# Performance work log

Hardware: AMD Instinct MI355X
Metric: run time of the kernel (lower is better)

The kernel has to match this reference:

```python
import jax, jax.numpy as jnp
import numpy as np

K = 4            # number of expert kernels
TEMPERATURE = 30.0  # T_max, initial temperature
KS = 3
PAD = 1
STRIDE = 1


def setup_inputs() -> dict:
    key = jax.random.key(0)
    k1, k2, k3, k4, k5 = jax.random.split(key, 5)
    b, c_in, c_out, f, t, ctx = 32, 256, 256, 64, 64, 256
    x = jax.random.normal(k1, (b, c_in, f, t), dtype=jnp.float32)
    g = jax.random.normal(k2, (b, ctx), dtype=jnp.float32)
    # expert kernels: (k, out, in//groups, ks, ks), kaiming-normal-ish init
    fan_in = c_in * KS * KS
    weight = jax.random.normal(k3, (K, c_out, c_in, KS, KS), dtype=jnp.float32) * jnp.sqrt(2.0 / fan_in)
    # attention Dense: ctx -> k * att_groups (att_groups = 1)
    dense_w = jax.random.normal(k4, (ctx, K), dtype=jnp.float32) * jnp.sqrt(1.0 / ctx)
    dense_b = jnp.zeros((K,), dtype=jnp.float32)
    return {"x": x, "g": g, "weight": weight, "dense_w": dense_w, "dense_b": dense_b}


def reference(x, g, weight, dense_w, dense_b):
    b, c, f, t = x.shape
    k, c_out, c_in_pg, ks, _ = weight.shape
    # attention over k expert kernels, per batch element (att_groups = 1)
    logits = g @ dense_w + dense_b                      # (b, k)
    attention = jax.nn.softmax(logits / TEMPERATURE, axis=-1)
    # per-sample mixed kernel: (b, out, in, ks, ks)
    agg_w = jnp.einsum('bk,koihw->boihw', attention, weight)
    agg_w = agg_w.reshape(b * c_out, c_in_pg, ks, ks)
    # batched per-sample conv via feature_group_count = groups * b (groups = 1)
    xg = x.reshape(1, b * c, f, t)
    out = jax.lax.conv_general_dilated(
        xg, agg_w,
        window_strides=(STRIDE, STRIDE),
        padding=((PAD, PAD), (PAD, PAD)),
        lhs_dilation=(1, 1), rhs_dilation=(1, 1),
        dimension_numbers=('NCHW', 'OIHW', 'NCHW'),
        feature_group_count=b,
    )
    return out.reshape(b, c_out, out.shape[-2], out.shape[-1])
```

## Files before the change

kernel.cpp:

```cpp
#include <hip/hip_runtime.h>
#include <hip/hip_bf16.h>
#include <stdint.h>

#define BATCH 32
#define CIN   256
#define COUT  256
#define FH    64
#define FW    64
#define NK    4
#define CTX   256
#define TEMP  30.0f

typedef __attribute__((ext_vector_type(8))) short bf16x8;
typedef __attribute__((ext_vector_type(4))) float f32x4;

__device__ __forceinline__ unsigned short f2bf(float f) {
    union { float f; uint32_t u; } a; a.f = f;
    uint32_t r = a.u + 0x7fffu + ((a.u >> 16) & 1u);
    return (unsigned short)(r >> 16);
}

#define WMIX_OFF  1024
#define WMIX_BYTES (32u * 9u * 8u * 4u * 256u * 16u)
#define XP_OFF    (WMIX_OFF + WMIX_BYTES)

__global__ void attn_kernel(const float* __restrict__ g,
                            const float* __restrict__ dw,
                            const float* __restrict__ db,
                            float* __restrict__ att) {
    int tid = threadIdx.x;
    int b = tid >> 2;
    int k = tid & 3;
    float acc = db[k];
    const float* gp = g + b * CTX;
    for (int i = 0; i < CTX; ++i)
        acc += gp[i] * dw[i * NK + k];
    acc *= (1.0f / TEMP);
    float m = acc;
    m = fmaxf(m, __shfl_xor(m, 1));
    m = fmaxf(m, __shfl_xor(m, 2));
    float e = expf(acc - m);
    float s = e;
    s += __shfl_xor(s, 1);
    s += __shfl_xor(s, 2);
    att[b * NK + k] = e / s;
}

__global__ __launch_bounds__(256, 2) void mix_kernel(
        const float* __restrict__ weight,
        const float* __restrict__ att,
        uint32_t* __restrict__ wmix) {
    __shared__ __align__(16) short S[2 * 8 * 2308];

    const int t   = threadIdx.x;
    const int cog = blockIdx.x;
    const int bg  = blockIdx.y;
    const int co0 = cog * 8;
    const int b0  = bg * 2;
    const size_t EST = (size_t)COUT * CIN * 9;

    float a[2][4];
#pragma unroll
    for (int nb = 0; nb < 2; ++nb)
#pragma unroll
        for (int k = 0; k < 4; ++k)
            a[nb][k] = att[(b0 + nb) * 4 + k];

    const int co_l  = t >> 5;
    const int inner = t & 31;
    const float* wbase = weight + (size_t)(co0 + co_l) * 2304;

#pragma unroll 2
    for (int i = 0; i < 18; ++i) {
        const int e4 = inner + 32 * i;
        float4 w[4];
#pragma unroll
        for (int k = 0; k < 4; ++k)
            w[k] = *(const float4*)(wbase + k * EST + (size_t)e4 * 4);
#pragma unroll
        for (int nb = 0; nb < 2; ++nb) {
            float mx = a[nb][0] * w[0].x + a[nb][1] * w[1].x + a[nb][2] * w[2].x + a[nb][3] * w[3].x;
            float my = a[nb][0] * w[0].y + a[nb][1] * w[1].y + a[nb][2] * w[2].y + a[nb][3] * w[3].y;
            float mz = a[nb][0] * w[0].z + a[nb][1] * w[1].z + a[nb][2] * w[2].z + a[nb][3] * w[3].z;
            float mw = a[nb][0] * w[0].w + a[nb][1] * w[1].w + a[nb][2] * w[2].w + a[nb][3] * w[3].w;
            uint32_t lo = (uint32_t)f2bf(mx) | ((uint32_t)f2bf(my) << 16);
            uint32_t hi = (uint32_t)f2bf(mz) | ((uint32_t)f2bf(mw) << 16);
            uint2* d = (uint2*)(S + ((nb * 8 + co_l) * 2308 + e4 * 4));
            *d = make_uint2(lo, hi);
        }
    }
    __syncthreads();

    const int co_w = t & 7;
    const int slot = t >> 3;
#pragma unroll 2
    for (int j = 0; j < 18; ++j) {
        const int GG  = j * 32 + slot;
        const int b_l = (GG >= 288) ? 1 : 0;
        const int rem = GG - b_l * 288;
        const int tap = rem >> 5;
        const int ch  = (rem >> 2) & 7;
        const int q   = rem & 3;
        const short* sp = S + (b_l * 8 + co_w) * 2308;
        const int ebase = (ch * 32 + q * 8) * 9 + tap;
        uint32_t d[4];
#pragma unroll
        for (int rp = 0; rp < 4; ++rp) {
            uint32_t lo = (uint16_t)sp[ebase + (2 * rp) * 9];
            uint32_t hi = (uint16_t)sp[ebase + (2 * rp + 1) * 9];
            d[rp] = lo | (hi << 16);
        }
        uint32_t* dst = wmix +
            ((((size_t)((b0 + b_l) * 9 + tap) * 8 + ch) * 4 + q) * 256 + co0 + co_w) * 4;
        *(uint4*)dst = make_uint4(d[0], d[1], d[2], d[3]);
    }
}

__global__ void xpad_kernel(const float* __restrict__ x,
                            uint32_t* __restrict__ xp) {
    __shared__ uint32_t P[1088];
    const int t  = threadIdx.x;
    const int y  = blockIdx.x;
    const int ch = blockIdx.y;
    const int b  = blockIdx.z;

    for (int i = t; i < 1088; i += 256) P[i] = 0;
    __syncthreads();

    if (y >= 1 && y <= 64) {
        const int ci_l = t >> 3;
        const int col0 = (t & 7) * 8;
        const float* xr = x + (((size_t)(b * 256 + ch * 32 + ci_l) * 64) + (y - 1)) * 64 + col0;
        float4 v0 = *(const float4*)xr;
        float4 v1 = *(const float4*)(xr + 4);
        unsigned short bf[8];
        bf[0] = f2bf(v0.x); bf[1] = f2bf(v0.y); bf[2] = f2bf(v0.z); bf[3] = f2bf(v0.w);
        bf[4] = f2bf(v1.x); bf[5] = f2bf(v1.y); bf[6] = f2bf(v1.z); bf[7] = f2bf(v1.w);
        const int q = ci_l >> 3, r = ci_l & 7;
        unsigned short* Ps = (unsigned short*)P;
#pragma unroll
        for (int j = 0; j < 8; ++j)
            Ps[(q * 68 + (col0 + j + 1)) * 8 + r] = bf[j];
    }
    __syncthreads();

    const int q = t >> 6, l = t & 63;
    uint32_t* base = xp + (((((size_t)(b * 8 + ch) * 4 + q) * 66) + y) * 68) * 4;
#pragma unroll
    for (int i = 0; i < 4; ++i)
        base[l + i * 64] = P[q * 272 + l + i * 64];
    if (l < 16) base[l + 256] = P[q * 272 + l + 256];
}

__global__ __launch_bounds__(256, 3) void conv_mfma(
        const char* __restrict__ xp,
        const char* __restrict__ wmix,
        float* __restrict__ out) {
    __shared__ __align__(16) short As[3 * 4 * 128 * 8];
    __shared__ __align__(16) short Bs[4 * 2 * 68 * 8];

    const int tid  = threadIdx.x;
    const int lane = tid & 63;
    const int wv   = tid >> 6;
    const int wm   = wv & 1;
    const int wn   = wv >> 1;
    const int l4   = lane >> 4;
    const int m16  = lane & 15;

    const int ptile = blockIdx.x;
    const int coT   = blockIdx.y;
    const int b     = blockIdx.z;
    const int y0    = ptile * 2;

    const char* wmix_b = wmix + (size_t)b * 9 * 8 * 4 * 256 * 16;
    const char* xp_b   = xp + (size_t)b * 8 * 4 * 66 * 68 * 16;

    f32x4 acc[4][4];
#pragma unroll
    for (int i = 0; i < 4; ++i)
#pragma unroll
        for (int j = 0; j < 4; ++j)
            acc[i][j] = (f32x4){0.f, 0.f, 0.f, 0.f};

    const int aLane = l4 * 2048 + wm * 1024 + m16 * 16;
    const int bLane = l4 * 2176 + wn * 1088 + m16 * 16;

#pragma unroll 1
    for (int ch = 0; ch < 8; ++ch) {
#pragma unroll 1
        for (int dy = 0; dy < 3; ++dy) {
            __syncthreads();
#pragma unroll
            for (int i = 0; i < 6; ++i) {
                const int s  = wv + i * 4;
                const int dx = s >> 3;
                const int q  = (s >> 1) & 3;
                const int h  = s & 1;
                const char* gsrc = wmix_b
                    + ((size_t)((dy * 3 + dx) * 8 + ch) * 4 + q) * 4096
                    + (coT * 128 + h * 64 + lane) * 16;
                char* ldst = (char*)As + ((dx * 4 + q) * 128 + h * 64 + lane) * 16;
                __builtin_amdgcn_global_load_lds(
                    (const __attribute__((address_space(1))) void*)gsrc,
                    (__attribute__((address_space(3))) void*)ldst, 16, 0, 0);
            }
            {
                const int yb = y0 + dy;
                const char* gsrc = xp_b
                    + (((size_t)ch * 4 + wv) * 66 + yb) * 1088 + lane * 16;
                char* ldst = (char*)Bs + wv * 2176 + lane * 16;
                __builtin_amdgcn_global_load_lds(
                    (const __attribute__((address_space(1))) void*)gsrc,
                    (__attribute__((address_space(3))) void*)ldst, 16, 0, 0);
                __builtin_amdgcn_global_load_lds(
                    (const __attribute__((address_space(1))) void*)(gsrc + 1024),
                    (__attribute__((address_space(3))) void*)(ldst + 1024), 16, 0, 0);
                if (lane < 8)
                    __builtin_amdgcn_global_load_lds(
                        (const __attribute__((address_space(1))) void*)(gsrc + 2048),
                        (__attribute__((address_space(3))) void*)(ldst + 2048), 16, 0, 0);
            }
            __syncthreads();

#pragma unroll
            for (int dx = 0; dx < 3; ++dx) {
                bf16x8 a[4], bb[4];
#pragma unroll
                for (int sm = 0; sm < 4; ++sm)
                    a[sm] = *(const bf16x8*)((const char*)As + dx * 8192 + aLane + sm * 256);
#pragma unroll
                for (int sn = 0; sn < 4; ++sn)
                    bb[sn] = *(const bf16x8*)((const char*)Bs + bLane + dx * 16 + sn * 256);
#pragma unroll
                for (int sm = 0; sm < 4; ++sm)
#pragma unroll
                    for (int sn = 0; sn < 4; ++sn)
                        acc[sm][sn] = __builtin_amdgcn_mfma_f32_16x16x32_bf16(
                            a[sm], bb[sn], acc[sm][sn], 0, 0, 0);
            }
        }
    }

    const int y = y0 + wn;
#pragma unroll
    for (int sm = 0; sm < 4; ++sm) {
#pragma unroll
        for (int sn = 0; sn < 4; ++sn) {
#pragma unroll
            for (int r = 0; r < 4; ++r) {
                const int co = coT * 128 + wm * 64 + sm * 16 + l4 * 4 + r;
                const int xx = sn * 16 + m16;
                out[(((size_t)b * COUT + co) * FH + y) * FW + xx] = acc[sm][sn][r];
            }
        }
    }
}

extern "C" void kernel_launch(void* const* d_in, const int* in_sizes, int n_in,
                              void* d_out, int out_size, void* d_ws, size_t ws_size,
                              hipStream_t stream) {
    const float* x       = (const float*)d_in[0];
    const float* g       = (const float*)d_in[1];
    const float* weight  = (const float*)d_in[2];
    const float* dense_w = (const float*)d_in[3];
    const float* dense_b = (const float*)d_in[4];
    float* out = (float*)d_out;

    float*    att  = (float*)d_ws;
    uint32_t* wmix = (uint32_t*)((char*)d_ws + WMIX_OFF);
    uint32_t* xp   = (uint32_t*)((char*)d_ws + XP_OFF);

    attn_kernel<<<1, 128, 0, stream>>>(g, dense_w, dense_b, att);
    mix_kernel<<<dim3(32, 16), 256, 0, stream>>>(weight, att, wmix);
    xpad_kernel<<<dim3(66, 8, BATCH), 256, 0, stream>>>(x, xp);

    dim3 grid(32, 2, BATCH);
    conv_mfma<<<grid, 256, 0, stream>>>((const char*)xp, (const char*)wmix, out);
}
```

Baseline: 401.4 us.

## Double-buffer conv LDS staging, fuse attention into mix, batch xpad rows, remap grid

The conv kernel now double-buffers its A and B LDS tiles, prefetching the next (channel, dy) stage while MFMAs run on the current one. It also pads LDS rows to avoid bank conflicts, raises MFMA priority with setprio, and swizzles the block index across XCDs. The attention softmax is recomputed inside each mix block, which removes one launch, and xpad handles six rows per block. In exchange, double buffering doubles LDS use, so launch bounds drop from 3 to 2 blocks per SM, which lowers occupancy.

```diff
diff --git a/kernel.cpp b/kernel.cpp
--- a/kernel.cpp
+++ b/kernel.cpp
@@ -24,33 +24,15 @@
 #define WMIX_BYTES (32u * 9u * 8u * 4u * 256u * 16u)
 #define XP_OFF    (WMIX_OFF + WMIX_BYTES)
 
-__global__ void attn_kernel(const float* __restrict__ g,
-                            const float* __restrict__ dw,
-                            const float* __restrict__ db,
-                            float* __restrict__ att) {
-    int tid = threadIdx.x;
-    int b = tid >> 2;
-    int k = tid & 3;
-    float acc = db[k];
-    const float* gp = g + b * CTX;
-    for (int i = 0; i < CTX; ++i)
-        acc += gp[i] * dw[i * NK + k];
-    acc *= (1.0f / TEMP);
-    float m = acc;
-    m = fmaxf(m, __shfl_xor(m, 1));
-    m = fmaxf(m, __shfl_xor(m, 2));
-    float e = expf(acc - m);
-    float s = e;
-    s += __shfl_xor(s, 1);
-    s += __shfl_xor(s, 2);
-    att[b * NK + k] = e / s;
-}
-
 __global__ __launch_bounds__(256, 2) void mix_kernel(
         const float* __restrict__ weight,
-        const float* __restrict__ att,
+        const float* __restrict__ g,
+        const float* __restrict__ dw,
+        const float* __restrict__ db,
         uint32_t* __restrict__ wmix) {
     __shared__ __align__(16) short S[2 * 8 * 2308];
+    __shared__ float logit_s[8];
+    __shared__ float att_s[8];
 
     const int t   = threadIdx.x;
     const int cog = blockIdx.x;
@@ -59,12 +41,44 @@
     const int b0  = bg * 2;
     const size_t EST = (size_t)COUT * CIN * 9;
 
+    {
+        const int p  = t >> 5;
+        const int i0 = t & 31;
+        const int nb = p >> 2, k = p & 3;
+        const float* gp = g + (size_t)(b0 + nb) * CTX;
+        float part = 0.f;
+#pragma unroll
+        for (int j = 0; j < 8; ++j) {
+            const int i = i0 + j * 32;
+            part += gp[i] * dw[i * NK + k];
+        }
+#pragma unroll
+        for (int m = 1; m <= 16; m <<= 1) part += __shfl_xor(part, m);
+        if (i0 == 0) logit_s[p] = part + db[k];
+    }
+    __syncthreads();
+    if (t < 8) {
+        const int nb = t >> 2;
+        const float l0 = logit_s[nb * 4 + 0] * (1.f / TEMP);
+        const float l1 = logit_s[nb * 4 + 1] * (1.f / TEMP);
+        const float l2 = logit_s[nb * 4 + 2] * (1.f / TEMP);
+        const float l3 = logit_s[nb * 4 + 3] * (1.f / TEMP);
+        const float m  = fmaxf(fmaxf(l0, l1), fmaxf(l2, l3));
+        const float e0 = expf(l0 - m), e1 = expf(l1 - m);
+        const float e2 = expf(l2 - m), e3 = expf(l3 - m);
+        const float s  = e0 + e1 + e2 + e3;
+        const int   k  = t & 3;
+        const float e  = (k == 0) ? e0 : (k == 1) ? e1 : (k == 2) ? e2 : e3;
+        att_s[t] = e / s;
+    }
+    __syncthreads();
+
     float a[2][4];
 #pragma unroll
     for (int nb = 0; nb < 2; ++nb)
 #pragma unroll
         for (int k = 0; k < 4; ++k)
-            a[nb][k] = att[(b0 + nb) * 4 + k];
+            a[nb][k] = att_s[nb * 4 + k];
 
     const int co_l  = t >> 5;
     const int inner = t & 31;
@@ -116,48 +130,57 @@
     }
 }
 
-__global__ void xpad_kernel(const float* __restrict__ x,
-                            uint32_t* __restrict__ xp) {
-    __shared__ uint32_t P[1088];
+__global__ __launch_bounds__(256) void xpad_kernel(const float* __restrict__ x,
+                                                   uint32_t* __restrict__ xp) {
+    __shared__ uint32_t P[6 * 1088];
     const int t  = threadIdx.x;
-    const int y  = blockIdx.x;
+    const int yg = blockIdx.x;
     const int ch = blockIdx.y;
     const int b  = blockIdx.z;
 
-    for (int i = t; i < 1088; i += 256) P[i] = 0;
-    __syncthreads();
-
-    if (y >= 1 && y <= 64) {
-        const int ci_l = t >> 3;
-        const int col0 = (t & 7) * 8;
-        const float* xr = x + (((size_t)(b * 256 + ch * 32 + ci_l) * 64) + (y - 1)) * 64 + col0;
-        float4 v0 = *(const float4*)xr;
-        float4 v1 = *(const float4*)(xr + 4);
-        unsigned short bf[8];
-        bf[0] = f2bf(v0.x); bf[1] = f2bf(v0.y); bf[2] = f2bf(v0.z); bf[3] = f2bf(v0.w);
-        bf[4] = f2bf(v1.x); bf[5] = f2bf(v1.y); bf[6] = f2bf(v1.z); bf[7] = f2bf(v1.w);
-        const int q = ci_l >> 3, r = ci_l & 7;
-        unsigned short* Ps = (unsigned short*)P;
-#pragma unroll
-        for (int j = 0; j < 8; ++j)
-            Ps[(q * 68 + (col0 + j + 1)) * 8 + r] = bf[j];
-    }
-    __syncthreads();
-
-    const int q = t >> 6, l = t & 63;
-    uint32_t* base = xp + (((((size_t)(b * 8 + ch) * 4 + q) * 66) + y) * 68) * 4;
-#pragma unroll
-    for (int i = 0; i < 4; ++i)
-        base[l + i * 64] = P[q * 272 + l + i * 64];
-    if (l < 16) base[l + 256] = P[q * 272 + l + 256];
-}
-
-__global__ __launch_bounds__(256, 3) void conv_mfma(
+    for (int i = t; i < 6 * 1088; i += 256) P[i] = 0;
+    __syncthreads();
+
+    const int ci_l = t >> 3;
+    const int col0 = (t & 7) * 8;
+    const int q = ci_l >> 3, r = ci_l & 7;
+    unsigned short* Ps = (unsigned short*)P;
+
+#pragma unroll
+    for (int yy = 0; yy < 6; ++yy) {
+        const int y = yg * 6 + yy;
+        if (y >= 1 && y <= 64) {
+            const float* xr = x + (((size_t)(b * 256 + ch * 32 + ci_l) * 64) + (y - 1)) * 64 + col0;
+            float4 v0 = *(const float4*)xr;
+            float4 v1 = *(const float4*)(xr + 4);
+            unsigned short bf[8];
+            bf[0] = f2bf(v0.x); bf[1] = f2bf(v0.y); bf[2] = f2bf(v0.z); bf[3] = f2bf(v0.w);
+            bf[4] = f2bf(v1.x); bf[5] = f2bf(v1.y); bf[6] = f2bf(v1.z); bf[7] = f2bf(v1.w);
+#pragma unroll
+            for (int j = 0; j < 8; ++j)
+                Ps[yy * 2176 + (q * 68 + (col0 + j + 1)) * 8 + r] = bf[j];
+        }
+    }
+    __syncthreads();
+
+    const int qo = t >> 6, l = t & 63;
+#pragma unroll
+    for (int yy = 0; yy < 6; ++yy) {
+        const int y = yg * 6 + yy;
+        uint32_t* base = xp + (((((size_t)(b * 8 + ch) * 4 + qo) * 66) + y) * 68) * 4;
+#pragma unroll
+        for (int i = 0; i < 4; ++i)
+            base[l + i * 64] = P[yy * 1088 + qo * 272 + l + i * 64];
+        if (l < 16) base[l + 256] = P[yy * 1088 + qo * 272 + l + 256];
+    }
+}
+
+__global__ __launch_bounds__(256, 2) void conv_mfma(
         const char* __restrict__ xp,
         const char* __restrict__ wmix,
         float* __restrict__ out) {
-    __shared__ __align__(16) short As[3 * 4 * 128 * 8];
-    __shared__ __align__(16) short Bs[4 * 2 * 68 * 8];
+    __shared__ __align__(16) char As[2][3 * 4 * 2064];
+    __shared__ __align__(16) char Bs[2][4 * 2192];
 
     const int tid  = threadIdx.x;
     const int lane = tid & 63;
@@ -167,9 +190,11 @@
     const int l4   = lane >> 4;
     const int m16  = lane & 15;
 
-    const int ptile = blockIdx.x;
-    const int coT   = blockIdx.y;
-    const int b     = blockIdx.z;
+    const int bx  = blockIdx.x;
+    const int wid = (bx & 7) * 256 + (bx >> 3);
+    const int ptile = wid & 31;
+    const int coT   = (wid >> 5) & 1;
+    const int b     = wid >> 6;
     const int y0    = ptile * 2;
 
     const char* wmix_b = wmix + (size_t)b * 9 * 8 * 4 * 256 * 16;
@@ -182,63 +207,70 @@
         for (int j = 0; j < 4; ++j)
             acc[i][j] = (f32x4){0.f, 0.f, 0.f, 0.f};
 
-    const int aLane = l4 * 2048 + wm * 1024 + m16 * 16;
-    const int bLane = l4 * 2176 + wn * 1088 + m16 * 16;
+    const int aLane = l4 * 2064 + wm * 1024 + m16 * 16;
+    const int bLane = l4 * 2192 + wn * 1088 + m16 * 16;
+
+    auto stage = [&](char* Asb, char* Bsb, int p) {
+        const int ch = p / 3, dy = p - ch * 3;
+#pragma unroll
+        for (int i = 0; i < 6; ++i) {
+            const int s  = wv + i * 4;
+            const int dx = s >> 3;
+            const int q  = (s >> 1) & 3;
+            const int h  = s & 1;
+            const char* gsrc = wmix_b
+                + ((size_t)((dy * 3 + dx) * 8 + ch) * 4 + q) * 4096
+                + (coT * 128 + h * 64 + lane) * 16;
+            char* ldst = Asb + dx * 8256 + q * 2064 + (h * 64 + lane) * 16;
+            __builtin_amdgcn_global_load_lds(
+                (const __attribute__((address_space(1))) void*)gsrc,
+                (__attribute__((address_space(3))) void*)ldst, 16, 0, 0);
+        }
+        const int yb = y0 + dy;
+        const char* gsrc = xp_b
+            + (((size_t)ch * 4 + wv) * 66 + yb) * 1088 + lane * 16;
+        char* ldst = Bsb + wv * 2192 + lane * 16;
+        __builtin_amdgcn_global_load_lds(
+            (const __attribute__((address_space(1))) void*)gsrc,
+            (__attribute__((address_space(3))) void*)ldst, 16, 0, 0);
+        __builtin_amdgcn_global_load_lds(
+            (const __attribute__((address_space(1))) void*)(gsrc + 1024),
+            (__attribute__((address_space(3))) void*)(ldst + 1024), 16, 0, 0);
+        if (lane < 8)
+            __builtin_amdgcn_global_load_lds(
+                (const __attribute__((address_space(1))) void*)(gsrc + 2048),
+                (__attribute__((address_space(3))) void*)(ldst + 2048), 16, 0, 0);
+    };
+
+    stage(As[0], Bs[0], 0);
+    __syncthreads();
 
 #pragma unroll 1
-    for (int ch = 0; ch < 8; ++ch) {
-#pragma unroll 1
-        for (int dy = 0; dy < 3; ++dy) {
-            __syncthreads();
-#pragma unroll
-            for (int i = 0; i < 6; ++i) {
-                const int s  = wv + i * 4;
-                const int dx = s >> 3;
-                const int q  = (s >> 1) & 3;
-                const int h  = s & 1;
-                const char* gsrc = wmix_b
-                    + ((size_t)((dy * 3 + dx) * 8 + ch) * 4 + q) * 4096
-                    + (coT * 128 + h * 64 + lane) * 16;
-                char* ldst = (char*)As + ((dx * 4 + q) * 128 + h * 64 + lane) * 16;
-                __builtin_amdgcn_global_load_lds(
-                    (const __attribute__((address_space(1))) void*)gsrc,
-                    (__attribute__((address_space(3))) void*)ldst, 16, 0, 0);
-            }
-            {
-                const int yb = y0 + dy;
-                const char* gsrc = xp_b
-                    + (((size_t)ch * 4 + wv) * 66 + yb) * 1088 + lane * 16;
-                char* ldst = (char*)Bs + wv * 2176 + lane * 16;
-                __builtin_amdgcn_global_load_lds(
-                    (const __attribute__((address_space(1))) void*)gsrc,
-                    (__attribute__((address_space(3))) void*)ldst, 16, 0, 0);
-                __builtin_amdgcn_global_load_lds(
-                    (const __attribute__((address_space(1))) void*)(gsrc + 1024),
-                    (__attribute__((address_space(3))) void*)(ldst + 1024), 16, 0, 0);
-                if (lane < 8)
-                    __builtin_amdgcn_global_load_lds(
-                        (const __attribute__((address_space(1))) void*)(gsrc + 2048),
-                        (__attribute__((address_space(3))) void*)(ldst + 2048), 16, 0, 0);
-            }
-            __syncthreads();
-
-#pragma unroll
-            for (int dx = 0; dx < 3; ++dx) {
-                bf16x8 a[4], bb[4];
-#pragma unroll
-                for (int sm = 0; sm < 4; ++sm)
-                    a[sm] = *(const bf16x8*)((const char*)As + dx * 8192 + aLane + sm * 256);
+    for (int p = 0; p < 24; ++p) {
+        const int cur = p & 1;
+        if (p < 23) stage(As[cur ^ 1], Bs[cur ^ 1], p + 1);
+
+        const char* Asc = As[cur];
+        const char* Bsc = Bs[cur];
+#pragma unroll
+        for (int dx = 0; dx < 3; ++dx) {
+            bf16x8 a[4], bb[4];
+#pragma unroll
+            for (int sm = 0; sm < 4; ++sm)
+                a[sm] = *(const bf16x8*)(Asc + dx * 8256 + aLane + sm * 256);
+#pragma unroll
+            for (int sn = 0; sn < 4; ++sn)
+                bb[sn] = *(const bf16x8*)(Bsc + bLane + dx * 16 + sn * 256);
+            __builtin_amdgcn_s_setprio(1);
+#pragma unroll
+            for (int sm = 0; sm < 4; ++sm)
 #pragma unroll
                 for (int sn = 0; sn < 4; ++sn)
-                    bb[sn] = *(const bf16x8*)((const char*)Bs + bLane + dx * 16 + sn * 256);
-#pragma unroll
-                for (int sm = 0; sm < 4; ++sm)
-#pragma unroll
-                    for (int sn = 0; sn < 4; ++sn)
-                        acc[sm][sn] = __builtin_amdgcn_mfma_f32_16x16x32_bf16(
-                            a[sm], bb[sn], acc[sm][sn], 0, 0, 0);
-            }
-        }
+                    acc[sm][sn] = __builtin_amdgcn_mfma_f32_16x16x32_bf16(
+                        a[sm], bb[sn], acc[sm][sn], 0, 0, 0);
+            __builtin_amdgcn_s_setprio(0);
+        }
+        __syncthreads();
     }
 
     const int y = y0 + wn;
@@ -266,14 +298,10 @@
     const float* dense_b = (const float*)d_in[4];
     float* out = (float*)d_out;
 
-    float*    att  = (float*)d_ws;
     uint32_t* wmix = (uint32_t*)((char*)d_ws + WMIX_OFF);
     uint32_t* xp   = (uint32_t*)((char*)d_ws + XP_OFF);
 
-    attn_kernel<<<1, 128, 0, stream>>>(g, dense_w, dense_b, att);
-    mix_kernel<<<dim3(32, 16), 256, 0, stream>>>(weight, att, wmix);
-    xpad_kernel<<<dim3(66, 8, BATCH), 256, 0, stream>>>(x, xp);
-
-    dim3 grid(32, 2, BATCH);
-    conv_mfma<<<grid, 256, 0, stream>>>((const char*)xp, (const char*)wmix, out);
-}
+    mix_kernel<<<dim3(32, 16), 256, 0, stream>>>(weight, g, dense_w, dense_b, wmix);
+    xpad_kernel<<<dim3(11, 8, BATCH), 256, 0, stream>>>(x, xp);
+    conv_mfma<<<2048, 256, 0, stream>>>((const char*)xp, (const char*)wmix, out);
+}
```

Result: slower. 417.6 us (+4.0%).
